# Optimization experiments

Hardware: AMD Instinct MI355X
Metric: run time of the kernel (lower is better)

Reference implementation:

```python
import jax, jax.numpy as jnp
import numpy as np

B = 8192
E = 8
H = 128
NUM_CLASSES = 3
SIM_THRESHOLD = 0.8
EFF_THRESHOLD = 0.1
TARGET_TEMP = 1.0
W_LB, W_EFF, W_CONS, W_ENT, W_TEMP = 0.1, 0.05, 0.1, 0.01, 0.01


def setup_inputs() -> dict:
    key = jax.random.key(0)
    k1, k2, k3, k4 = jax.random.split(key, 4)
    logits = jax.random.normal(k1, (B, NUM_CLASSES), dtype=jnp.float32)
    targets = jax.random.randint(k2, (B,), 0, NUM_CLASSES, dtype=jnp.int64)
    raw = jax.random.uniform(k3, (B, E), dtype=jnp.float32)
    routing_probs = raw / raw.sum(axis=-1, keepdims=True)  # rows sum to 1
    input_embeddings = jax.random.uniform(k4, (B, H), dtype=jnp.float32)
    temperature = jnp.ones((1,), dtype=jnp.float32)
    return {
        "logits": logits,
        "targets": targets,
        "routing_probs": routing_probs,
        "input_embeddings": input_embeddings,
        "temperature": temperature,
    }


def _dynamo_loss(logits, routing_probs, input_embeddings, temperature, targets):
    # --- task loss: cross entropy (sentiment) ---
    logp_cls = jax.nn.log_softmax(logits, axis=-1)
    task_loss = -jnp.take_along_axis(logp_cls, targets[:, None], axis=-1).mean()

    # --- load balance: var(mean usage) / (1/E)^2 (torch.var unbiased) ---
    expert_usage = routing_probs.mean(axis=0)  # [E]
    lb_loss = W_LB * jnp.var(expert_usage, ddof=1) * (E ** 2)

    # --- efficiency: sum of probs below threshold, averaged over batch ---
    small = jnp.where(routing_probs < EFF_THRESHOLD, routing_probs, 0.0)
    eff_loss = W_EFF * small.sum(axis=-1).mean()

    # --- consistency: masked pairwise KL over similar samples ---
    nrm = input_embeddings / jnp.linalg.norm(input_embeddings, axis=-1, keepdims=True)
    sim = nrm @ nrm.T  # [B, B]
    mask = (sim > SIM_THRESHOLD) & ~jnp.eye(B, dtype=bool)
    logp = jax.nn.log_softmax(routing_probs, axis=-1)  # [B, E]
    p = jnp.exp(logp)
    a = jnp.sum(p * logp, axis=-1)  # [B], sum_e p_j log p_j
    # KL(i,j) = sum_e p_j (log p_j - log p_i) = a[j] - logp[i] . p[j]
    kl = a[None, :] - logp @ p.T  # [B, B]
    num_pairs = mask.sum()
    kl_sum = jnp.sum(jnp.where(mask, kl, 0.0))
    cons_loss = W_CONS * jnp.where(num_pairs > 0, kl_sum / jnp.maximum(num_pairs, 1), 0.0)

    # --- entropy regularization (maximize entropy of routing_probs-as-probs) ---
    eps = 1e-8
    entropy = -jnp.sum(routing_probs * jnp.log(routing_probs + eps), axis=-1)
    ent_loss = W_ENT * (-entropy.mean())

    # --- temperature regularization ---
    temp_loss = W_TEMP * jnp.mean((temperature - TARGET_TEMP) ** 2)

    return task_loss + lb_loss + eff_loss + cons_loss + ent_loss + temp_loss


def reference(logits, targets, routing_probs, input_embeddings, temperature):
    return _dynamo_loss(logits, routing_probs, input_embeddings, temperature, targets)
```

## Files before the change

### kernel.cpp

```cpp
#include <hip/hip_runtime.h>
#include <stdint.h>

#define B_SZ 8192
#define LOG8 2.0794415416798357f
#define NTILE 2080

typedef __attribute__((ext_vector_type(8))) short short8;
typedef __attribute__((ext_vector_type(4))) float floatx4;

__device__ inline unsigned short f2bf(float f) {
    unsigned int u = __float_as_uint(f);
    u = (u + 0x7FFFu + ((u >> 16) & 1u)) >> 16;
    return (unsigned short)u;
}
__device__ inline float bf2f(unsigned short s) {
    return __uint_as_float(((unsigned int)s) << 16);
}
__device__ inline float wredf(float x) {
#pragma unroll
    for (int o = 32; o; o >>= 1) x += __shfl_down(x, o);
    return x;
}
__device__ inline int wredi(int x) {
#pragma unroll
    for (int o = 32; o; o >>= 1) x += __shfl_down(x, o);
    return x;
}

__global__ void prep_all(const float* __restrict__ logits,
                         const int* __restrict__ targets,
                         const float* __restrict__ routing,
                         const float* __restrict__ emb,
                         unsigned short* __restrict__ nrm,
                         unsigned short* __restrict__ lq,
                         unsigned short* __restrict__ pb,
                         float* __restrict__ aprime,
                         float* __restrict__ acc) {
    const int bid = blockIdx.x;
    const int lane = threadIdx.x & 63;

    if (bid < 2048) {
        int wave = threadIdx.x >> 6;
        int row = (bid << 2) + wave;
        const float2* e2 = (const float2*)(emb + (size_t)row * 128);
        float2 v = e2[lane];
        float ss = v.x * v.x + v.y * v.y;
        ss = wredf(ss);
        ss = __shfl(ss, 0);
        float inv = rsqrtf(ss);
        ushort2 o;
        o.x = f2bf(v.x * inv);
        o.y = f2bf(v.y * inv);
        ((ushort2*)(nrm + (size_t)row * 128))[lane] = o;
        return;
    }

    int row = ((bid - 2048) << 8) + threadIdx.x;

    const float4* r4 = (const float4*)(routing + (size_t)row * 8);
    float4 va = r4[0], vb = r4[1];
    float v[8] = {va.x, va.y, va.z, va.w, vb.x, vb.y, vb.z, vb.w};

    float mx = v[0];
#pragma unroll
    for (int e = 1; e < 8; ++e) mx = fmaxf(mx, v[e]);
    float ex[8], s = 0.f;
#pragma unroll
    for (int e = 0; e < 8; ++e) { ex[e] = expf(v[e] - mx); s += ex[e]; }
    float ls = logf(s);
    float inv_s = 1.f / s;

    union { unsigned short u[8]; uint4 q; } lu, pu;
    float ap = 0.f;
#pragma unroll
    for (int e = 0; e < 8; ++e) {
        unsigned short pe = f2bf(ex[e] * inv_s);
        unsigned short le = f2bf(v[e] - mx - ls + LOG8);
        pu.u[e] = pe;
        lu.u[e] = le;
        ap += bf2f(pe) * bf2f(le);
    }
    ((uint4*)lq)[row] = lu.q;
    ((uint4*)pb)[row] = pu.q;
    aprime[row] = ap;

    float eff = 0.f, ent = 0.f;
#pragma unroll
    for (int e = 0; e < 8; ++e) {
        if (v[e] < 0.1f) eff += v[e];
        ent += v[e] * logf(v[e] + 1e-8f);
    }

    const float* lg = logits + (size_t)row * 3;
    float a0 = lg[0], a1 = lg[1], a2 = lg[2];
    float mm = fmaxf(a0, fmaxf(a1, a2));
    float lse = mm + logf(expf(a0 - mm) + expf(a1 - mm) + expf(a2 - mm));
    int tg = targets[row];
    float tv = (tg == 0) ? a0 : ((tg == 1) ? a1 : a2);
    float task = lse - tv;

    task = wredf(task);
    eff = wredf(eff);
    ent = wredf(ent);
    float cs[8];
#pragma unroll
    for (int e = 0; e < 8; ++e) cs[e] = wredf(v[e]);

    if (lane == 0) {
        atomicAdd(&acc[0], task);
        atomicAdd(&acc[1], eff);
        atomicAdd(&acc[2], ent);
#pragma unroll
        for (int e = 0; e < 8; ++e) atomicAdd(&acc[4 + e], cs[e]);
    }
}

__global__ __launch_bounds__(512, 4) void tile_sym(
    const unsigned short* __restrict__ nrm,
    const unsigned short* __restrict__ lq,
    const unsigned short* __restrict__ pb,
    const float* __restrict__ aprime,
    float* __restrict__ acc) {
    __shared__ uint4 sh[2][128][16];

    const int t = threadIdx.x;
    const int L = blockIdx.x;

    int bi = (int)((129.0f - sqrtf((float)(16641 - 8 * L))) * 0.5f);
    int T = bi * 64 - ((bi * (bi - 1)) >> 1);
    while (L < T) { --bi; T = bi * 64 - ((bi * (bi - 1)) >> 1); }
    while (L >= T + (64 - bi)) { T += 64 - bi; ++bi; }
    const int bj = bi + (L - T);
    const bool diag = (bi == bj);
    const int iBase = bi << 7, jBase = bj << 7;

    const uint4* n4 = (const uint4*)nrm;
#pragma unroll
    for (int it = 0; it < 4; ++it) {
        int c = t + (it << 9);
        int row = c >> 4, g = c & 15;
        int gp = g ^ (row & 15);
        uint4 va = n4[((size_t)(iBase + row) << 4) + g];
        uint4 vb = n4[((size_t)(jBase + row) << 4) + g];
        sh[0][row][gp] = va;
        sh[1][row][gp] = vb;
    }

    const int wave = t >> 6, lane = t & 63;
    const int wr = wave >> 2, wc = wave & 3;
    const int m = lane & 15, q = lane >> 4;

    const short8 zero8 = (short8){0, 0, 0, 0, 0, 0, 0, 0};
    short8 crA[4], crB[2];
    float apB[2];
    float apA[4][4];
    const unsigned short* baseA = q ? pb : lq;
    const unsigned short* baseB = q ? lq : pb;
#pragma unroll
    for (int a = 0; a < 4; ++a) {
        int ri = iBase + (wr << 6) + (a << 4) + m;
        short8 v = zero8;
        if (q < 2) v = *(const short8*)&baseA[(size_t)ri << 3];
        if (diag && q == 1) v = zero8;
        crA[a] = v;
        float4 a4 = *(const float4*)&aprime[iBase + (wr << 6) + (a << 4) + (q << 2)];
        apA[a][0] = a4.x; apA[a][1] = a4.y; apA[a][2] = a4.z; apA[a][3] = a4.w;
    }
#pragma unroll
    for (int b = 0; b < 2; ++b) {
        int cj = jBase + (wc << 5) + (b << 4) + m;
        short8 v = zero8;
        if (q < 2) v = *(const short8*)&baseB[(size_t)cj << 3];
        if (diag && q == 1) v = zero8;
        crB[b] = v;
        apB[b] = aprime[cj];
    }

    __syncthreads();

    const unsigned short* Ab = (const unsigned short*)&sh[0][0][0];
    const unsigned short* Bb = (const unsigned short*)&sh[1][0][0];

    floatx4 simacc[4][2];
#pragma unroll
    for (int a = 0; a < 4; ++a)
#pragma unroll
        for (int b = 0; b < 2; ++b) simacc[a][b] = (floatx4){0.f, 0.f, 0.f, 0.f};

#pragma unroll
    for (int ks = 0; ks < 4; ++ks) {
        const int g = (ks << 2) + q;
        short8 af[4], bfr[2];
#pragma unroll
        for (int a = 0; a < 4; ++a) {
            int ra = (wr << 6) + (a << 4) + m;
            af[a] = *(const short8*)&Ab[(ra << 7) + ((g ^ m) << 3)];
        }
#pragma unroll
        for (int b = 0; b < 2; ++b) {
            int rb = (wc << 5) + (b << 4) + m;
            bfr[b] = *(const short8*)&Bb[(rb << 7) + ((g ^ m) << 3)];
        }
#pragma unroll
        for (int a = 0; a < 4; ++a)
#pragma unroll
            for (int b = 0; b < 2; ++b)
                simacc[a][b] = __builtin_amdgcn_mfma_f32_16x16x32_bf16(
                    af[a], bfr[b], simacc[a][b], 0, 0, 0);
    }

    float klLocal = 0.f;
    int cntLocal = 0;
#pragma unroll
    for (int a = 0; a < 4; ++a) {
        const int gRow0 = iBase + (wr << 6) + (a << 4) + (q << 2);
#pragma unroll
        for (int b = 0; b < 2; ++b) {
            const int gCol = jBase + (wc << 5) + (b << 4) + m;
            floatx4 cr = __builtin_amdgcn_mfma_f32_16x16x32_bf16(
                crA[a], crB[b], (floatx4){0.f, 0.f, 0.f, 0.f}, 0, 0, 0);
            if (diag) {
#pragma unroll
                for (int r = 0; r < 4; ++r) {
                    if ((simacc[a][b][r] > 0.8f) && (gRow0 + r != gCol)) {
                        klLocal += apB[b] - cr[r];
                        cntLocal += 1;
                    }
                }
            } else {
#pragma unroll
                for (int r = 0; r < 4; ++r) {
                    if (simacc[a][b][r] > 0.8f) {
                        klLocal += apA[a][r] + apB[b] - cr[r];
                        cntLocal += 2;
                    }
                }
            }
        }
    }

    klLocal = wredf(klLocal);
    cntLocal = wredi(cntLocal);

    __syncthreads();
    float* redk = (float*)&sh[0][0][0];
    int* redc = (int*)(redk + 8);
    if (lane == 0) { redk[wave] = klLocal; redc[wave] = cntLocal; }
    __syncthreads();

    if (t == 0) {
        float k = 0.f;
        int c = 0;
#pragma unroll
        for (int w = 0; w < 8; ++w) { k += redk[w]; c += redc[w]; }
        int slot = L & 63;
        atomicAdd(&acc[16 + slot], k);
        atomicAdd(&((unsigned int*)acc)[80 + slot], (unsigned int)c);
    }
}

__global__ void finalize_k(const float* __restrict__ acc,
                           const float* __restrict__ temp,
                           float* __restrict__ out) {
    int lane = threadIdx.x;
    float k = acc[16 + lane];
    int c = (int)((const unsigned int*)acc)[80 + lane];
    k = wredf(k);
    c = wredi(c);
    if (lane == 0) {
        const float invB = 1.f / (float)B_SZ;
        float task = acc[0] * invB;
        float eff = 0.05f * acc[1] * invB;
        float entl = 0.01f * acc[2] * invB;
        float cons = 0.1f * (c > 0 ? k / (float)c : 0.f);
        float u[8], mean = 0.f;
        for (int e = 0; e < 8; ++e) { u[e] = acc[4 + e] * invB; mean += u[e]; }
        mean *= 0.125f;
        float var = 0.f;
        for (int e = 0; e < 8; ++e) { float d = u[e] - mean; var += d * d; }
        var *= (1.f / 7.f);
        float lb = 0.1f * var * 64.f;
        float tt = temp[0] - 1.f;
        out[0] = task + lb + eff + cons + entl + 0.01f * tt * tt;
    }
}

extern "C" void kernel_launch(void* const* d_in, const int* in_sizes, int n_in,
                              void* d_out, int out_size, void* d_ws, size_t ws_size,
                              hipStream_t stream) {
    const float* logits = (const float*)d_in[0];
    const int* targets = (const int*)d_in[1];
    const float* routing = (const float*)d_in[2];
    const float* emb = (const float*)d_in[3];
    const float* temp = (const float*)d_in[4];

    char* ws = (char*)d_ws;
    unsigned short* nrm = (unsigned short*)ws;
    unsigned short* lq = (unsigned short*)(ws + 2097152);
    unsigned short* pb = (unsigned short*)(ws + 2228224);
    float* aprime = (float*)(ws + 2359296);
    float* acc = (float*)(ws + 2392064);

    hipMemsetAsync(acc, 0, 1024, stream);
    prep_all<<<2080, 256, 0, stream>>>(logits, targets, routing, emb,
                                       nrm, lq, pb, aprime, acc);
    tile_sym<<<NTILE, 512, 0, stream>>>(nrm, lq, pb, aprime, acc);
    finalize_k<<<1, 64, 0, stream>>>(acc, temp, (float*)d_out);
}
```

Before: 116.5 us.

## Process four tiles per block with prefetch, fold aprime into MFMA, drop atomics

Each tile_sym block now walks four consecutive upper-triangular tiles. It reuses the row-block embeddings in shared memory when bi does not change and prefetches the next column block into registers while the current tile computes. The aprime terms and the sign of the log-prob dot product are folded into the small KL MFMA by storing negated log-probs and packing aprime and ones into spare lanes, which removes per-element adds. Global atomics and the memset are replaced by per-block slot writes reduced in a wider finalize kernel. The risks are one-quarter as many blocks (520) on the GPU, hence lower parallelism, and extra syncs per tile.

```diff
diff --git a/kernel.cpp b/kernel.cpp
--- a/kernel.cpp
+++ b/kernel.cpp
@@ -4,6 +4,7 @@
 #define B_SZ 8192
 #define LOG8 2.0794415416798357f
 #define NTILE 2080
+#define NCHUNK 520
 
 typedef __attribute__((ext_vector_type(8))) short short8;
 typedef __attribute__((ext_vector_type(4))) float floatx4;
@@ -26,21 +27,23 @@
     for (int o = 32; o; o >>= 1) x += __shfl_down(x, o);
     return x;
 }
+
 
 __global__ void prep_all(const float* __restrict__ logits,
                          const int* __restrict__ targets,
                          const float* __restrict__ routing,
                          const float* __restrict__ emb,
                          unsigned short* __restrict__ nrm,
-                         unsigned short* __restrict__ lq,
+                         unsigned short* __restrict__ nlq,
                          unsigned short* __restrict__ pb,
                          float* __restrict__ aprime,
-                         float* __restrict__ acc) {
+                         float* __restrict__ prepslot) {
+    __shared__ float pred[4][11];
     const int bid = blockIdx.x;
     const int lane = threadIdx.x & 63;
+    const int wave = threadIdx.x >> 6;
 
     if (bid < 2048) {
-        int wave = threadIdx.x >> 6;
         int row = (bid << 2) + wave;
         const float2* e2 = (const float2*)(emb + (size_t)row * 128);
         float2 v = e2[lane];
@@ -77,10 +80,10 @@
         unsigned short pe = f2bf(ex[e] * inv_s);
         unsigned short le = f2bf(v[e] - mx - ls + LOG8);
         pu.u[e] = pe;
-        lu.u[e] = le;
+        lu.u[e] = le ^ 0x8000;
         ap += bf2f(pe) * bf2f(le);
     }
-    ((uint4*)lq)[row] = lu.q;
+    ((uint4*)nlq)[row] = lu.q;
     ((uint4*)pb)[row] = pu.q;
     aprime[row] = ap;
 
@@ -107,136 +110,181 @@
     for (int e = 0; e < 8; ++e) cs[e] = wredf(v[e]);
 
     if (lane == 0) {
-        atomicAdd(&acc[0], task);
-        atomicAdd(&acc[1], eff);
-        atomicAdd(&acc[2], ent);
-#pragma unroll
-        for (int e = 0; e < 8; ++e) atomicAdd(&acc[4 + e], cs[e]);
+        pred[wave][0] = task;
+        pred[wave][1] = eff;
+        pred[wave][2] = ent;
+#pragma unroll
+        for (int e = 0; e < 8; ++e) pred[wave][3 + e] = cs[e];
+    }
+    __syncthreads();
+    if (threadIdx.x < 11) {
+        prepslot[(bid - 2048) * 11 + threadIdx.x] =
+            pred[0][threadIdx.x] + pred[1][threadIdx.x] +
+            pred[2][threadIdx.x] + pred[3][threadIdx.x];
     }
 }
 
 __global__ __launch_bounds__(512, 4) void tile_sym(
     const unsigned short* __restrict__ nrm,
-    const unsigned short* __restrict__ lq,
+    const unsigned short* __restrict__ nlq,
     const unsigned short* __restrict__ pb,
     const float* __restrict__ aprime,
-    float* __restrict__ acc) {
+    float* __restrict__ klslot,
+    unsigned int* __restrict__ cntslot) {
     __shared__ uint4 sh[2][128][16];
 
     const int t = threadIdx.x;
-    const int L = blockIdx.x;
-
-    int bi = (int)((129.0f - sqrtf((float)(16641 - 8 * L))) * 0.5f);
+    const int L0 = blockIdx.x << 2;
+
+    int bi = (int)((129.0f - sqrtf((float)(16641 - 8 * L0))) * 0.5f);
     int T = bi * 64 - ((bi * (bi - 1)) >> 1);
-    while (L < T) { --bi; T = bi * 64 - ((bi * (bi - 1)) >> 1); }
-    while (L >= T + (64 - bi)) { T += 64 - bi; ++bi; }
-    const int bj = bi + (L - T);
-    const bool diag = (bi == bj);
-    const int iBase = bi << 7, jBase = bj << 7;
+    while (L0 < T) { --bi; T = bi * 64 - ((bi * (bi - 1)) >> 1); }
+    while (L0 >= T + (64 - bi)) { T += 64 - bi; ++bi; }
+    int bj = bi + (L0 - T);
 
     const uint4* n4 = (const uint4*)nrm;
-#pragma unroll
-    for (int it = 0; it < 4; ++it) {
-        int c = t + (it << 9);
-        int row = c >> 4, g = c & 15;
-        int gp = g ^ (row & 15);
-        uint4 va = n4[((size_t)(iBase + row) << 4) + g];
-        uint4 vb = n4[((size_t)(jBase + row) << 4) + g];
-        sh[0][row][gp] = va;
-        sh[1][row][gp] = vb;
-    }
-
     const int wave = t >> 6, lane = t & 63;
     const int wr = wave >> 2, wc = wave & 3;
     const int m = lane & 15, q = lane >> 4;
-
     const short8 zero8 = (short8){0, 0, 0, 0, 0, 0, 0, 0};
-    short8 crA[4], crB[2];
-    float apB[2];
-    float apA[4][4];
-    const unsigned short* baseA = q ? pb : lq;
-    const unsigned short* baseB = q ? lq : pb;
-#pragma unroll
-    for (int a = 0; a < 4; ++a) {
-        int ri = iBase + (wr << 6) + (a << 4) + m;
-        short8 v = zero8;
-        if (q < 2) v = *(const short8*)&baseA[(size_t)ri << 3];
-        if (diag && q == 1) v = zero8;
-        crA[a] = v;
-        float4 a4 = *(const float4*)&aprime[iBase + (wr << 6) + (a << 4) + (q << 2)];
-        apA[a][0] = a4.x; apA[a][1] = a4.y; apA[a][2] = a4.z; apA[a][3] = a4.w;
-    }
-#pragma unroll
-    for (int b = 0; b < 2; ++b) {
-        int cj = jBase + (wc << 5) + (b << 4) + m;
-        short8 v = zero8;
-        if (q < 2) v = *(const short8*)&baseB[(size_t)cj << 3];
-        if (diag && q == 1) v = zero8;
-        crB[b] = v;
-        apB[b] = aprime[cj];
-    }
-
-    __syncthreads();
-
-    const unsigned short* Ab = (const unsigned short*)&sh[0][0][0];
-    const unsigned short* Bb = (const unsigned short*)&sh[1][0][0];
-
-    floatx4 simacc[4][2];
-#pragma unroll
-    for (int a = 0; a < 4; ++a)
-#pragma unroll
-        for (int b = 0; b < 2; ++b) simacc[a][b] = (floatx4){0.f, 0.f, 0.f, 0.f};
-
-#pragma unroll
-    for (int ks = 0; ks < 4; ++ks) {
-        const int g = (ks << 2) + q;
-        short8 af[4], bfr[2];
-#pragma unroll
-        for (int a = 0; a < 4; ++a) {
-            int ra = (wr << 6) + (a << 4) + m;
-            af[a] = *(const short8*)&Ab[(ra << 7) + ((g ^ m) << 3)];
-        }
-#pragma unroll
-        for (int b = 0; b < 2; ++b) {
-            int rb = (wc << 5) + (b << 4) + m;
-            bfr[b] = *(const short8*)&Bb[(rb << 7) + ((g ^ m) << 3)];
-        }
-#pragma unroll
-        for (int a = 0; a < 4; ++a)
-#pragma unroll
-            for (int b = 0; b < 2; ++b)
-                simacc[a][b] = __builtin_amdgcn_mfma_f32_16x16x32_bf16(
-                    af[a], bfr[b], simacc[a][b], 0, 0, 0);
-    }
 
     float klLocal = 0.f;
     int cntLocal = 0;
-#pragma unroll
-    for (int a = 0; a < 4; ++a) {
-        const int gRow0 = iBase + (wr << 6) + (a << 4) + (q << 2);
+    int prev_bi = -1;
+    uint4 bpre[4];
+
+#pragma unroll 1
+    for (int tt = 0; tt < 4; ++tt) {
+        const bool diag = (bi == bj);
+        const int iBase = bi << 7, jBase = bj << 7;
+
+        if (tt == 0) {
+#pragma unroll
+            for (int it = 0; it < 4; ++it) {
+                int cc = t + (it << 9);
+                int row = cc >> 4, g = cc & 15;
+                int gp = g ^ (row & 15);
+                sh[0][row][gp] = n4[((size_t)(iBase + row) << 4) + g];
+                sh[1][row][gp] = n4[((size_t)(jBase + row) << 4) + g];
+            }
+        } else {
+            __syncthreads();
+#pragma unroll
+            for (int it = 0; it < 4; ++it) {
+                int cc = t + (it << 9);
+                int row = cc >> 4, g = cc & 15;
+                sh[1][row][g ^ (row & 15)] = bpre[it];
+            }
+            if (bi != prev_bi) {
+#pragma unroll
+                for (int it = 0; it < 4; ++it) {
+                    int cc = t + (it << 9);
+                    int row = cc >> 4, g = cc & 15;
+                    sh[0][row][g ^ (row & 15)] = n4[((size_t)(iBase + row) << 4) + g];
+                }
+            }
+        }
+        __syncthreads();
+
+        int nbi = bi, nbj = bj + 1;
+        if (nbj == 64) { nbi = bi + 1; nbj = nbi; }
+        if (tt < 3) {
+#pragma unroll
+            for (int it = 0; it < 4; ++it) {
+                int cc = t + (it << 9);
+                int row = cc >> 4, g = cc & 15;
+                bpre[it] = n4[((size_t)((nbj << 7) + row) << 4) + g];
+            }
+        }
+
+        short8 crA[4], crB[2];
+#pragma unroll
+        for (int a = 0; a < 4; ++a) {
+            int ri = iBase + (wr << 6) + (a << 4) + m;
+            short8 v = zero8;
+            if (q == 0) v = *(const short8*)&nlq[(size_t)ri << 3];
+            else if (q == 1) { if (!diag) v = *(const short8*)&pb[(size_t)ri << 3]; }
+            else if (q == 2) {
+                v[1] = (short)0x3F80;
+                if (!diag) v[0] = (short)f2bf(aprime[ri]);
+            }
+            crA[a] = v;
+        }
 #pragma unroll
         for (int b = 0; b < 2; ++b) {
-            const int gCol = jBase + (wc << 5) + (b << 4) + m;
-            floatx4 cr = __builtin_amdgcn_mfma_f32_16x16x32_bf16(
-                crA[a], crB[b], (floatx4){0.f, 0.f, 0.f, 0.f}, 0, 0, 0);
-            if (diag) {
-#pragma unroll
-                for (int r = 0; r < 4; ++r) {
-                    if ((simacc[a][b][r] > 0.8f) && (gRow0 + r != gCol)) {
-                        klLocal += apB[b] - cr[r];
-                        cntLocal += 1;
+            int cj = jBase + (wc << 5) + (b << 4) + m;
+            short8 v = zero8;
+            if (q == 0) v = *(const short8*)&pb[(size_t)cj << 3];
+            else if (q == 1) v = *(const short8*)&nlq[(size_t)cj << 3];
+            else if (q == 2) {
+                v[0] = (short)0x3F80;
+                v[1] = (short)f2bf(aprime[cj]);
+            }
+            crB[b] = v;
+        }
+
+        const unsigned short* Ab = (const unsigned short*)&sh[0][0][0];
+        const unsigned short* Bb = (const unsigned short*)&sh[1][0][0];
+
+        floatx4 simacc[4][2];
+#pragma unroll
+        for (int a = 0; a < 4; ++a)
+#pragma unroll
+            for (int b = 0; b < 2; ++b) simacc[a][b] = (floatx4){0.f, 0.f, 0.f, 0.f};
+
+#pragma unroll
+        for (int ks = 0; ks < 4; ++ks) {
+            const int g = (ks << 2) + q;
+            short8 af[4], bfr[2];
+#pragma unroll
+            for (int a = 0; a < 4; ++a) {
+                int ra = (wr << 6) + (a << 4) + m;
+                af[a] = *(const short8*)&Ab[(ra << 7) + ((g ^ m) << 3)];
+            }
+#pragma unroll
+            for (int b = 0; b < 2; ++b) {
+                int rb = (wc << 5) + (b << 4) + m;
+                bfr[b] = *(const short8*)&Bb[(rb << 7) + ((g ^ m) << 3)];
+            }
+#pragma unroll
+            for (int a = 0; a < 4; ++a)
+#pragma unroll
+                for (int b = 0; b < 2; ++b)
+                    simacc[a][b] = __builtin_amdgcn_mfma_f32_16x16x32_bf16(
+                        af[a], bfr[b], simacc[a][b], 0, 0, 0);
+        }
+
+#pragma unroll
+        for (int a = 0; a < 4; ++a) {
+            const int gRow0 = iBase + (wr << 6) + (a << 4) + (q << 2);
+#pragma unroll
+            for (int b = 0; b < 2; ++b) {
+                const int gCol = jBase + (wc << 5) + (b << 4) + m;
+                floatx4 cr = __builtin_amdgcn_mfma_f32_16x16x32_bf16(
+                    crA[a], crB[b], (floatx4){0.f, 0.f, 0.f, 0.f}, 0, 0, 0);
+                if (diag) {
+#pragma unroll
+                    for (int r = 0; r < 4; ++r) {
+                        if ((simacc[a][b][r] > 0.8f) && (gRow0 + r != gCol)) {
+                            klLocal += cr[r];
+                            cntLocal += 1;
+                        }
+                    }
+                } else {
+#pragma unroll
+                    for (int r = 0; r < 4; ++r) {
+                        if (simacc[a][b][r] > 0.8f) {
+                            klLocal += cr[r];
+                            cntLocal += 2;
+                        }
                     }
                 }
-            } else {
-#pragma unroll
-                for (int r = 0; r < 4; ++r) {
-                    if (simacc[a][b][r] > 0.8f) {
-                        klLocal += apA[a][r] + apB[b] - cr[r];
-                        cntLocal += 2;
-                    }
-                }
-            }
-        }
+            }
+        }
+
+        prev_bi = bi;
+        bi = nbi;
+        bj = nbj;
     }
 
     klLocal = wredf(klLocal);
@@ -253,28 +301,43 @@
         int c = 0;
 #pragma unroll
         for (int w = 0; w < 8; ++w) { k += redk[w]; c += redc[w]; }
-        int slot = L & 63;
-        atomicAdd(&acc[16 + slot], k);
-        atomicAdd(&((unsigned int*)acc)[80 + slot], (unsigned int)c);
-    }
-}
-
-__global__ void finalize_k(const float* __restrict__ acc,
+        klslot[blockIdx.x] = k;
+        cntslot[blockIdx.x] = (unsigned int)c;
+    }
+}
+
+__global__ void finalize_k(const float* __restrict__ klslot,
+                           const unsigned int* __restrict__ cntslot,
+                           const float* __restrict__ prepslot,
                            const float* __restrict__ temp,
                            float* __restrict__ out) {
-    int lane = threadIdx.x;
-    float k = acc[16 + lane];
-    int c = (int)((const unsigned int*)acc)[80 + lane];
+    __shared__ float sk[4];
+    __shared__ int sc[4];
+    __shared__ float sp[11];
+    const int t = threadIdx.x, lane = t & 63, wave = t >> 6;
+
+    float k = 0.f;
+    int c = 0;
+    for (int i = t; i < NCHUNK; i += 256) { k += klslot[i]; c += (int)cntslot[i]; }
     k = wredf(k);
     c = wredi(c);
-    if (lane == 0) {
+    if (lane == 0) { sk[wave] = k; sc[wave] = c; }
+    if (t < 11) {
+        float s = 0.f;
+        for (int r = 0; r < 32; ++r) s += prepslot[r * 11 + t];
+        sp[t] = s;
+    }
+    __syncthreads();
+    if (t == 0) {
+        float K = sk[0] + sk[1] + sk[2] + sk[3];
+        int C = sc[0] + sc[1] + sc[2] + sc[3];
         const float invB = 1.f / (float)B_SZ;
-        float task = acc[0] * invB;
-        float eff = 0.05f * acc[1] * invB;
-        float entl = 0.01f * acc[2] * invB;
-        float cons = 0.1f * (c > 0 ? k / (float)c : 0.f);
+        float task = sp[0] * invB;
+        float eff = 0.05f * sp[1] * invB;
+        float entl = 0.01f * sp[2] * invB;
+        float cons = 0.1f * (C > 0 ? K / (float)C : 0.f);
         float u[8], mean = 0.f;
-        for (int e = 0; e < 8; ++e) { u[e] = acc[4 + e] * invB; mean += u[e]; }
+        for (int e = 0; e < 8; ++e) { u[e] = sp[3 + e] * invB; mean += u[e]; }
         mean *= 0.125f;
         float var = 0.f;
         for (int e = 0; e < 8; ++e) { float d = u[e] - mean; var += d * d; }
@@ -296,14 +359,16 @@
 
     char* ws = (char*)d_ws;
     unsigned short* nrm = (unsigned short*)ws;
-    unsigned short* lq = (unsigned short*)(ws + 2097152);
+    unsigned short* nlq = (unsigned short*)(ws + 2097152);
     unsigned short* pb = (unsigned short*)(ws + 2228224);
     float* aprime = (float*)(ws + 2359296);
-    float* acc = (float*)(ws + 2392064);
-
-    hipMemsetAsync(acc, 0, 1024, stream);
+    float* klslot = (float*)(ws + 2392064);
+    unsigned int* cntslot = (unsigned int*)(ws + 2394144);
+    float* prepslot = (float*)(ws + 2396224);
+
     prep_all<<<2080, 256, 0, stream>>>(logits, targets, routing, emb,
-                                       nrm, lq, pb, aprime, acc);
-    tile_sym<<<NTILE, 512, 0, stream>>>(nrm, lq, pb, aprime, acc);
-    finalize_k<<<1, 64, 0, stream>>>(acc, temp, (float*)d_out);
-}
+                                       nrm, nlq, pb, aprime, prepslot);
+    tile_sym<<<NCHUNK, 512, 0, stream>>>(nrm, nlq, pb, aprime, klslot, cntslot);
+    finalize_k<<<1, 256, 0, stream>>>(klslot, cntslot, prepslot, temp,
+                                      (float*)d_out);
+}
```

Result: slower. 121.6 us (+4.4%).
